# Optimization experiments

Hardware: AMD Instinct MI355X
Metric: run time of the kernel (lower is better)

The kernel has to match this reference:

```python
import jax, jax.numpy as jnp
import numpy as np

B, S, D, H, C = 64, 512, 768, 768, 5


def setup_inputs() -> dict:
    key = jax.random.key(0)
    ks = jax.random.split(key, 7)
    return {
        "hidden_states": jax.random.normal(ks[0], (B, S, D), jnp.float32),
        "mask": jnp.ones((B, S), dtype=bool),
        # Dense(hidden_size, relu)
        "W1": jax.random.normal(ks[1], (D, H), jnp.float32) * 0.02,
        "b1": jnp.zeros((H,), jnp.float32),
        # CRF inner dense -> potentials over num_classes
        "W2": jax.random.normal(ks[2], (H, C), jnp.float32) * 0.02,
        "b2": jnp.zeros((C,), jnp.float32),
        # CRF transition matrix and boundary energies (tfa use_boundary=True)
        "chain_kernel": jax.random.normal(ks[3], (C, C), jnp.float32) * 0.1,
        "left_boundary": jax.random.normal(ks[4], (C,), jnp.float32) * 0.1,
        "right_boundary": jax.random.normal(ks[5], (C,), jnp.float32) * 0.1,
    }


def viterbi_decode(potentials, trans):
    """potentials: [B,S,C], trans: [C,C] -> decoded tags [B,S] int32."""
    pot_t = jnp.swapaxes(potentials, 0, 1)  # [S,B,C]

    def fwd_step(alpha, pot):
        scores = alpha[:, :, None] + trans[None]      # [B,C_prev,C_cur]
        bp = jnp.argmax(scores, axis=1)               # [B,C]
        alpha = jnp.max(scores, axis=1) + pot         # [B,C]
        return alpha, bp

    alpha, bps = jax.lax.scan(fwd_step, pot_t[0], pot_t[1:])  # bps: [S-1,B,C]
    last = jnp.argmax(alpha, axis=-1).astype(jnp.int32)       # [B]

    def back_step(tag, bp):
        prev = jnp.take_along_axis(bp, tag[:, None], axis=1)[:, 0].astype(jnp.int32)
        return prev, prev

    _, tags = jax.lax.scan(back_step, last, bps, reverse=True)  # [S-1,B]
    decoded = jnp.concatenate([jnp.swapaxes(tags, 0, 1), last[:, None]], axis=1)
    return decoded


def reference(hidden_states, mask, W1, b1, W2, b2, chain_kernel,
              left_boundary, right_boundary):
    # Dense + ReLU (dropout is identity at inference / training=False)
    h = jax.nn.relu(jnp.einsum('bsd,dh->bsh', hidden_states, W1) + b1)
    # CRF inner dense -> unary potentials
    pot = jnp.einsum('bsh,hc->bsc', h, W2) + b2
    # boundary energies at first / last timestep (mask is full-length here)
    pot = pot.at[:, 0].add(left_boundary).at[:, -1].add(right_boundary)
    seq_length = jnp.sum(mask.astype(jnp.int32), axis=1)
    decoded = viterbi_decode(pot, chain_kernel)
    return decoded, pot, seq_length, chain_kernel
```

## Files before the change

### kernel.cpp

```cpp
#include <hip/hip_runtime.h>

#define B_  64
#define S_  512
#define D_  768
#define H_  768
#define C_  5
#define M_  (B_ * S_)

typedef float f32x4 __attribute__((ext_vector_type(4)));
typedef short short8 __attribute__((ext_vector_type(8)));

#define W1T_ELEMS (D_ * H_)
#define XBF_ELEMS (M_ * D_)

#define PX_BLOCKS   (XBF_ELEMS / (256 * 8))
#define PW_BLOCKS   ((D_ / 32) * (H_ / 32))
#define PI_BLOCKS   ((M_ * C_ + 255) / 256)

__device__ __forceinline__ unsigned short f2bf(float f) {
    unsigned int u = __float_as_uint(f);
    u += 0x7FFFu + ((u >> 16) & 1u);
    return (unsigned short)(u >> 16);
}

__global__ __launch_bounds__(256) void prep_all_kernel(
    const float* __restrict__ X, const float* __restrict__ W1,
    const float* __restrict__ b2, const float* __restrict__ lb,
    const float* __restrict__ rb,
    unsigned short* __restrict__ xbf, unsigned short* __restrict__ w1t,
    float* __restrict__ pot)
{
    __shared__ float t[32][33];
    const int bid = blockIdx.x;
    const int tid = threadIdx.x;

    if (bid < PX_BLOCKS) {
        const size_t i0 = ((size_t)bid * 256 + tid) * 8;
        const float4 a = *(const float4*)(X + i0);
        const float4 b = *(const float4*)(X + i0 + 4);
        union { unsigned short u[8]; uint4 v; } o;
        o.u[0] = f2bf(a.x); o.u[1] = f2bf(a.y); o.u[2] = f2bf(a.z); o.u[3] = f2bf(a.w);
        o.u[4] = f2bf(b.x); o.u[5] = f2bf(b.y); o.u[6] = f2bf(b.z); o.u[7] = f2bf(b.w);
        *(uint4*)(xbf + i0) = o.v;
    } else if (bid < PX_BLOCKS + PW_BLOCKS) {
        const int b2i = bid - PX_BLOCKS;
        const int bx = b2i % (H_ / 32);
        const int by = b2i / (H_ / 32);
        const int lx = tid & 31, ly = tid >> 5;
        #pragma unroll
        for (int j = 0; j < 4; ++j)
            t[ly + 8 * j][lx] = W1[(by * 32 + ly + 8 * j) * H_ + bx * 32 + lx];
        __syncthreads();
        #pragma unroll
        for (int j = 0; j < 4; ++j)
            w1t[(size_t)(bx * 32 + ly + 8 * j) * D_ + by * 32 + lx] = f2bf(t[lx][ly + 8 * j]);
    } else {
        const int idx = (bid - PX_BLOCKS - PW_BLOCKS) * 256 + tid;
        if (idx < M_ * C_) {
            const int c = idx % C_;
            const int tt = (idx / C_) & (S_ - 1);
            float v = b2[c];
            if (tt == 0)      v += lb[c];
            if (tt == S_ - 1) v += rb[c];
            pot[idx] = v;
        }
    }
}

__global__ __launch_bounds__(256) void prep_w1_kernel(
    const float* __restrict__ W1, unsigned short* __restrict__ w1t)
{
    __shared__ float t[32][33];
    const int bx = blockIdx.x, by = blockIdx.y;
    const int lx = threadIdx.x & 31, ly = threadIdx.x >> 5;
    #pragma unroll
    for (int j = 0; j < 4; ++j)
        t[ly + 8 * j][lx] = W1[(by * 32 + ly + 8 * j) * H_ + bx * 32 + lx];
    __syncthreads();
    #pragma unroll
    for (int j = 0; j < 4; ++j)
        w1t[(size_t)(bx * 32 + ly + 8 * j) * D_ + by * 32 + lx] = f2bf(t[lx][ly + 8 * j]);
}

__global__ __launch_bounds__(256) void init_pot_kernel(
    const float* __restrict__ b2, const float* __restrict__ lb,
    const float* __restrict__ rb, float* __restrict__ pot)
{
    const int idx = blockIdx.x * 256 + threadIdx.x;
    if (idx < M_ * C_) {
        const int c = idx % C_;
        const int t = (idx / C_) & (S_ - 1);
        float v = b2[c];
        if (t == 0)      v += lb[c];
        if (t == S_ - 1) v += rb[c];
        pot[idx] = v;
    }
}

__device__ __forceinline__ void gload16(const void* g, void* l) {
    __builtin_amdgcn_global_load_lds(
        (const __attribute__((address_space(1))) unsigned int*)g,
        (__attribute__((address_space(3))) unsigned int*)l, 16, 0, 0);
}

__global__ __launch_bounds__(256) void gemm_bk64_kernel(
    const unsigned short* __restrict__ xbf,
    const unsigned short* __restrict__ w1t,
    const float* __restrict__ b1,
    const float* __restrict__ W2,
    float* __restrict__ pot)
{
    __shared__ __align__(16) unsigned short Asm[2][8192];
    __shared__ __align__(16) unsigned short Bsm[2][8192];

    const int tid  = threadIdx.x;
    const int lane = tid & 63, w = tid >> 6;
    const int wm   = w >> 1, wn = w & 1;
    const int i15  = lane & 15, quad = lane >> 4;

    const int bid = blockIdx.x;
    const int r8 = bid & 7, q8 = bid >> 3;
    const int nb = q8 % 6, mhi = q8 / 6;
    const int m0 = (mhi * 8 + r8) * 128;
    const int n0 = nb * 128;

    const unsigned short* gA[2];
    const unsigned short* gB[2];
    int lofs[2];
    #pragma unroll
    for (int i = 0; i < 2; ++i) {
        const int g = 2 * w + i;
        gA[i] = xbf + (size_t)(m0 + g * 16 + i15) * D_ + quad * 8;
        gB[i] = w1t + (size_t)(n0 + g * 16 + i15) * D_ + quad * 8;
        lofs[i] = g * 512;
    }

    f32x4 acc[4][4];
    #pragma unroll
    for (int mi = 0; mi < 4; ++mi)
        #pragma unroll
        for (int ni = 0; ni < 4; ++ni)
            acc[mi][ni] = (f32x4){0.f, 0.f, 0.f, 0.f};

    #pragma unroll
    for (int i = 0; i < 2; ++i) {
        gload16(gA[i],      &Asm[0][lofs[i]]);
        gload16(gA[i] + 32, &Asm[0][4096 + lofs[i]]);
        gload16(gB[i],      &Bsm[0][lofs[i]]);
        gload16(gB[i] + 32, &Bsm[0][4096 + lofs[i]]);
        gA[i] += 64; gB[i] += 64;
    }
    __syncthreads();

    #define KITERS (D_ / 64)
    for (int kt = 0; kt < KITERS; ++kt) {
        const int cur = kt & 1, nxt = cur ^ 1;

        if (kt + 1 < KITERS) {
            #pragma unroll
            for (int i = 0; i < 2; ++i) {
                gload16(gA[i],      &Asm[nxt][lofs[i]]);
                gload16(gA[i] + 32, &Asm[nxt][4096 + lofs[i]]);
                gload16(gB[i],      &Bsm[nxt][lofs[i]]);
                gload16(gB[i] + 32, &Bsm[nxt][4096 + lofs[i]]);
                gA[i] += 64; gB[i] += 64;
            }
        }

        #pragma unroll
        for (int c = 0; c < 2; ++c) {
            const int cb = c * 4096;
            short8 af[4], bfr[4];
            #pragma unroll
            for (int mi = 0; mi < 4; ++mi)
                af[mi] = *(const short8*)&Asm[cur][cb + (wm * 4 + mi) * 512 + quad * 128 + i15 * 8];
            #pragma unroll
            for (int ni = 0; ni < 4; ++ni)
                bfr[ni] = *(const short8*)&Bsm[cur][cb + (wn * 4 + ni) * 512 + quad * 128 + i15 * 8];
            #pragma unroll
            for (int ni = 0; ni < 4; ++ni)
                #pragma unroll
                for (int mi = 0; mi < 4; ++mi)
                    acc[mi][ni] = __builtin_amdgcn_mfma_f32_16x16x32_bf16(
                        af[mi], bfr[ni], acc[mi][ni], 0, 0, 0);
        }

        __syncthreads();
    }

    float* pp = (float*)&Asm[0][0];

    float b1v[4], w2v[4][C_];
    #pragma unroll
    for (int ni = 0; ni < 4; ++ni) {
        const int col = n0 + wn * 64 + ni * 16 + i15;
        b1v[ni] = b1[col];
        #pragma unroll
        for (int cc = 0; cc < C_; ++cc) w2v[ni][cc] = W2[col * C_ + cc];
    }

    #pragma unroll
    for (int mi = 0; mi < 4; ++mi) {
        float ps[4][C_];
        #pragma unroll
        for (int r = 0; r < 4; ++r)
            #pragma unroll
            for (int cc = 0; cc < C_; ++cc) ps[r][cc] = 0.f;

        #pragma unroll
        for (int ni = 0; ni < 4; ++ni)
            #pragma unroll
            for (int r = 0; r < 4; ++r) {
                float h = acc[mi][ni][r] + b1v[ni];
                h = h > 0.f ? h : 0.f;
                #pragma unroll
                for (int cc = 0; cc < C_; ++cc)
                    ps[r][cc] = fmaf(h, w2v[ni][cc], ps[r][cc]);
            }

        #pragma unroll
        for (int off = 1; off < 16; off <<= 1)
            #pragma unroll
            for (int r = 0; r < 4; ++r)
                #pragma unroll
                for (int cc = 0; cc < C_; ++cc)
                    ps[r][cc] += __shfl_xor(ps[r][cc], off, 64);

        if (i15 == 0) {
            #pragma unroll
            for (int r = 0; r < 4; ++r) {
                const int row = wm * 64 + mi * 16 + quad * 4 + r;
                #pragma unroll
                for (int cc = 0; cc < C_; ++cc)
                    pp[(wn * 128 + row) * C_ + cc] = ps[r][cc];
            }
        }
    }
    __syncthreads();

    for (int idx = tid; idx < 128 * C_; idx += 256) {
        const int row = idx / C_, cc = idx % C_;
        atomicAdd(&pot[(size_t)(m0 + row) * C_ + cc],
                  pp[row * C_ + cc] + pp[(128 + row) * C_ + cc]);
    }
}

__global__ __launch_bounds__(256) void gemm_bf16_kernel(
    const float* __restrict__ X,
    const unsigned short* __restrict__ w1t,
    const float* __restrict__ b1,
    const float* __restrict__ W2,
    float* __restrict__ pot)
{
    __shared__ __align__(16) float          Asm[128 * 32];
    __shared__ __align__(16) unsigned short Bsm[128 * 32];
    __shared__ float pp[2][128][C_];

    const int tid  = threadIdx.x;
    const int lane = tid & 63, w = tid >> 6;
    const int wm   = w >> 1, wn = w & 1;
    const int i15  = lane & 15, quad = lane >> 4;

    const int bid = blockIdx.x;
    const int r8 = bid & 7, q8 = bid >> 3;
    const int nb = q8 % 6, mhi = q8 / 6;
    const int m0 = (mhi * 8 + r8) * 128;
    const int n0 = nb * 128;

    const float* gA[4];
    float* lA[4];
    const unsigned short* gB[2];
    unsigned short* lB[2];
    #pragma unroll
    for (int i = 0; i < 4; ++i) {
        const int a = 4 * w + i, g = a >> 1, h = a & 1;
        gA[i] = X + (size_t)(m0 + g * 16 + i15) * D_ + (4 * h + quad) * 4;
        lA[i] = &Asm[g * 512 + h * 256];
    }
    #pragma unroll
    for (int i = 0; i < 2; ++i) {
        const int b = 2 * w + i;
        gB[i] = w1t + (size_t)(n0 + b * 16 + i15) * D_ + quad * 8;
        lB[i] = &Bsm[b * 512];
    }

    f32x4 acc[4][4];
    #pragma unroll
    for (int mi = 0; mi < 4; ++mi)
        #pragma unroll
        for (int ni = 0; ni < 4; ++ni)
            acc[mi][ni] = (f32x4){0.f, 0.f, 0.f, 0.f};

    for (int kt = 0; kt < D_ / 32; ++kt) {
        __syncthreads();
        #pragma unroll
        for (int i = 0; i < 4; ++i) { gload16(gA[i], lA[i]); gA[i] += 32; }
        #pragma unroll
        for (int i = 0; i < 2; ++i) { gload16(gB[i], lB[i]); gB[i] += 32; }
        __syncthreads();

        short8 af[4];
        #pragma unroll
        for (int mi = 0; mi < 4; ++mi) {
            const int row = wm * 64 + mi * 16 + i15;
            const int base = (row >> 4) * 512 + (row & 15) * 4 + quad * 128;
            const f32x4 lo = *(const f32x4*)&Asm[base];
            const f32x4 hi = *(const f32x4*)&Asm[base + 64];
            float f[8];
            *(f32x4*)&f[0] = lo; *(f32x4*)&f[4] = hi;
            union { short8 s; unsigned short u[8]; } cv;
            #pragma unroll
            for (int j = 0; j < 8; ++j) cv.u[j] = f2bf(f[j]);
            af[mi] = cv.s;
        }
        short8 bfr[4];
        #pragma unroll
        for (int ni = 0; ni < 4; ++ni) {
            const int row = wn * 64 + ni * 16 + i15;
            bfr[ni] = *(const short8*)&Bsm[(row >> 4) * 512 + quad * 128 + (row & 15) * 8];
        }
        #pragma unroll
        for (int ni = 0; ni < 4; ++ni)
            #pragma unroll
            for (int mi = 0; mi < 4; ++mi)
                acc[mi][ni] = __builtin_amdgcn_mfma_f32_16x16x32_bf16(
                    af[mi], bfr[ni], acc[mi][ni], 0, 0, 0);
    }

    float b1v[4], w2v[4][C_];
    #pragma unroll
    for (int ni = 0; ni < 4; ++ni) {
        const int col = n0 + wn * 64 + ni * 16 + i15;
        b1v[ni] = b1[col];
        #pragma unroll
        for (int cc = 0; cc < C_; ++cc) w2v[ni][cc] = W2[col * C_ + cc];
    }

    #pragma unroll
    for (int mi = 0; mi < 4; ++mi) {
        float ps[4][C_];
        #pragma unroll
        for (int r = 0; r < 4; ++r)
            #pragma unroll
            for (int cc = 0; cc < C_; ++cc) ps[r][cc] = 0.f;

        #pragma unroll
        for (int ni = 0; ni < 4; ++ni)
            #pragma unroll
            for (int r = 0; r < 4; ++r) {
                float h = acc[mi][ni][r] + b1v[ni];
                h = h > 0.f ? h : 0.f;
                #pragma unroll
                for (int cc = 0; cc < C_; ++cc)
                    ps[r][cc] = fmaf(h, w2v[ni][cc], ps[r][cc]);
            }

        #pragma unroll
        for (int off = 1; off < 16; off <<= 1)
            #pragma unroll
            for (int r = 0; r < 4; ++r)
                #pragma unroll
                for (int cc = 0; cc < C_; ++cc)
                    ps[r][cc] += __shfl_xor(ps[r][cc], off, 64);

        if (i15 == 0) {
            #pragma unroll
            for (int r = 0; r < 4; ++r) {
                const int row = wm * 64 + mi * 16 + quad * 4 + r;
                #pragma unroll
                for (int cc = 0; cc < C_; ++cc)
                    pp[wn][row][cc] = ps[r][cc];
            }
        }
    }
    __syncthreads();

    for (int idx = tid; idx < 128 * C_; idx += 256) {
        const int row = idx / C_, cc = idx % C_;
        atomicAdd(&pot[(size_t)(m0 + row) * C_ + cc],
                  pp[0][row][cc] + pp[1][row][cc]);
    }
}

#define FBK 8
#define FLDS 132
__global__ __launch_bounds__(256) void gemm_relu_pot_kernel(
    const float* __restrict__ X, const float* __restrict__ W1,
    const float* __restrict__ b1, const float* __restrict__ W2,
    float* __restrict__ pot)
{
    __shared__ float As[FBK * FLDS];
    __shared__ float Bs[FBK * FLDS];
    __shared__ float w2s[128][C_];

    const int tid = threadIdx.x;
    const int tx = tid & 15, ty = tid >> 4;
    const int m0 = blockIdx.y * 128, n0 = blockIdx.x * 128;

    for (int idx = tid; idx < 128 * C_; idx += 256)
        w2s[idx / C_][idx % C_] = W2[(n0 + idx / C_) * C_ + idx % C_];

    float acc[2][2][4][4];
    #pragma unroll
    for (int a = 0; a < 2; ++a)
        #pragma unroll
        for (int b = 0; b < 2; ++b)
            #pragma unroll
            for (int i = 0; i < 4; ++i)
                #pragma unroll
                for (int j = 0; j < 4; ++j) acc[a][b][i][j] = 0.f;

    const int arow = tid >> 1, aq = tid & 1;
    const int brow = tid >> 5, bq = tid & 31;
    const float* Aptr = X + (m0 + arow) * D_ + aq * 4;
    const float* Bptr = W1 + brow * H_ + n0 + bq * 4;

    for (int kt = 0; kt < D_; kt += FBK) {
        const float4 avv = *(const float4*)Aptr;
        const float4 bvv = *(const float4*)Bptr;
        __syncthreads();
        As[(aq * 4 + 0) * FLDS + arow] = avv.x;
        As[(aq * 4 + 1) * FLDS + arow] = avv.y;
        As[(aq * 4 + 2) * FLDS + arow] = avv.z;
        As[(aq * 4 + 3) * FLDS + arow] = avv.w;
        *(float4*)&Bs[brow * FLDS + bq * 4] = bvv;
        __syncthreads();
        #pragma unroll
        for (int k = 0; k < FBK; ++k) {
            const float4 a0 = *(const float4*)&As[k * FLDS + (ty << 2)];
            const float4 a1 = *(const float4*)&As[k * FLDS + 64 + (ty << 2)];
            const float4 b0 = *(const float4*)&Bs[k * FLDS + (tx << 2)];
            const float4 b1r = *(const float4*)&Bs[k * FLDS + 64 + (tx << 2)];
            const float ar[2][4] = {{a0.x,a0.y,a0.z,a0.w},{a1.x,a1.y,a1.z,a1.w}};
            const float br[2][4] = {{b0.x,b0.y,b0.z,b0.w},{b1r.x,b1r.y,b1r.z,b1r.w}};
            #pragma unroll
            for (int ri = 0; ri < 2; ++ri)
                #pragma unroll
                for (int i = 0; i < 4; ++i)
                    #pragma unroll
                    for (int rj = 0; rj < 2; ++rj)
                        #pragma unroll
                        for (int j = 0; j < 4; ++j)
                            acc[ri][rj][i][j] = fmaf(ar[ri][i], br[rj][j], acc[ri][rj][i][j]);
        }
        Aptr += FBK;
        Bptr += FBK * H_;
    }

    float ps[2][4][C_];
    #pragma unroll
    for (int ri = 0; ri < 2; ++ri)
        #pragma unroll
        for (int i = 0; i < 4; ++i)
            #pragma unroll
            for (int cc = 0; cc < C_; ++cc) ps[ri][i][cc] = 0.f;

    #pragma unroll
    for (int rj = 0; rj < 2; ++rj)
        #pragma unroll
        for (int j = 0; j < 4; ++j) {
            const int nl = rj * 64 + (tx << 2) + j;
            const float bj = b1[n0 + nl];
            float w2c[C_];
            #pragma unroll
            for (int cc = 0; cc < C_; ++cc) w2c[cc] = w2s[nl][cc];
            #pragma unroll
            for (int ri = 0; ri < 2; ++ri)
                #pragma unroll
                for (int i = 0; i < 4; ++i) {
                    float h = acc[ri][rj][i][j] + bj;
                    h = h > 0.f ? h : 0.f;
                    #pragma unroll
                    for (int cc = 0; cc < C_; ++cc)
                        ps[ri][i][cc] = fmaf(h, w2c[cc], ps[ri][i][cc]);
                }
        }

    #pragma unroll
    for (int off = 1; off < 16; off <<= 1)
        #pragma unroll
        for (int ri = 0; ri < 2; ++ri)
            #pragma unroll
            for (int i = 0; i < 4; ++i)
                #pragma unroll
                for (int cc = 0; cc < C_; ++cc)
                    ps[ri][i][cc] += __shfl_xor(ps[ri][i][cc], off, 64);

    if (tx == 0)
        #pragma unroll
        for (int ri = 0; ri < 2; ++ri)
            #pragma unroll
            for (int i = 0; i < 4; ++i) {
                const int m = m0 + ri * 64 + (ty << 2) + i;
                #pragma unroll
                for (int cc = 0; cc < C_; ++cc)
                    atomicAdd(&pot[m * C_ + cc], ps[ri][i][cc]);
            }
}

__global__ __launch_bounds__(64) void viterbi_kernel(
    const float* __restrict__ pot, const float* __restrict__ trans,
    const int* __restrict__ mask, float* __restrict__ decoded,
    float* __restrict__ seqlen, float* __restrict__ chain_out)
{
    const int b = blockIdx.x;
    const int lane = threadIdx.x;

    __shared__ float pl[S_ * C_];
    __shared__ unsigned int bpk[S_];
    __shared__ unsigned int gseg[64];
    __shared__ int bt[64];
    __shared__ int dec_s[S_];
    __shared__ int s_last;

    const float* pb = pot + b * (S_ * C_);
    for (int i = lane; i < S_ * C_; i += 64) pl[i] = pb[i];

    int mcnt = 0;
    const int* mb = mask + b * S_;
    for (int i = lane; i < S_; i += 64) mcnt += (mb[i] != 0) ? 1 : 0;
    #pragma unroll
    for (int off = 32; off >= 1; off >>= 1) mcnt += __shfl_xor(mcnt, off, 64);

    if (b == 0 && lane < C_ * C_) chain_out[lane] = trans[lane];

    float tr[C_][C_];
    #pragma unroll
    for (int p = 0; p < C_; ++p)
        #pragma unroll
        for (int c = 0; c < C_; ++c) tr[p][c] = trans[p * C_ + c];

    __syncthreads();

    const float NEG = -1.0e30f;

    float G[C_][C_];
    #pragma unroll
    for (int c = 0; c < C_; ++c)
        #pragma unroll
        for (int p = 0; p < C_; ++p) G[c][p] = (c == p) ? 0.f : NEG;

    for (int j = 1; j <= 8; ++j) {
        const int t = 8 * lane + j;
        if (t < S_) {
            float ng[C_][C_];
            #pragma unroll
            for (int c = 0; c < C_; ++c) {
                const float pc = pl[t * C_ + c];
                #pragma unroll
                for (int p = 0; p < C_; ++p) {
                    float m = tr[0][c] + G[0][p];
                    #pragma unroll
                    for (int q = 1; q < C_; ++q)
                        m = fmaxf(m, tr[q][c] + G[q][p]);
                    ng[c][p] = m + pc;
                }
            }
            #pragma unroll
            for (int c = 0; c < C_; ++c)
                #pragma unroll
                for (int p = 0; p < C_; ++p) G[c][p] = ng[c][p];
        }
    }

    #pragma unroll
    for (int d = 1; d < 64; d <<= 1) {
        float Q[C_][C_];
        #pragma unroll
        for (int q = 0; q < C_; ++q)
            #pragma unroll
            for (int p = 0; p < C_; ++p) Q[q][p] = __shfl_up(G[q][p], d, 64);
        if (lane >= d) {
            float ng[C_][C_];
            #pragma unroll
            for (int c = 0; c < C_; ++c)
                #pragma unroll
                for (int p = 0; p < C_; ++p) {
                    float m = G[c][0] + Q[0][p];
                    #pragma unroll
                    for (int q = 1; q < C_; ++q)
                        m = fmaxf(m, G[c][q] + Q[q][p]);
                    ng[c][p] = m;
                }
            #pragma unroll
            for (int c = 0; c < C_; ++c)
                #pragma unroll
                for (int p = 0; p < C_; ++p) G[c][p] = ng[c][p];
        }
    }

    float a[C_];
    {
        float E[C_][C_];
        #pragma unroll
        for (int c = 0; c < C_; ++c)
            #pragma unroll
            for (int p = 0; p < C_; ++p) E[c][p] = __shfl_up(G[c][p], 1, 64);
        float a0[C_];
        #pragma unroll
        for (int c = 0; c < C_; ++c) a0[c] = pl[c];
        if (lane == 0) {
            #pragma unroll
            for (int c = 0; c < C_; ++c) a[c] = a0[c];
        } else {
            #pragma unroll
            for (int c = 0; c < C_; ++c) {
                float m = E[c][0] + a0[0];
                #pragma unroll
                for (int q = 1; q < C_; ++q) m = fmaxf(m, E[c][q] + a0[q]);
                a[c] = m;
            }
        }
    }

    for (int j = 1; j <= 8; ++j) {
        const int t = 8 * lane + j;
        if (t < S_) {
            unsigned int mpack = 0;
            float na[C_];
            #pragma unroll
            for (int c = 0; c < C_; ++c) {
                float best = a[0] + tr[0][c];
                int arg = 0;
                #pragma unroll
                for (int p = 1; p < C_; ++p) {
                    const float s = a[p] + tr[p][c];
                    if (s > best) { best = s; arg = p; }
                }
                mpack |= (unsigned int)arg << (3 * c);
                na[c] = best + pl[t * C_ + c];
            }
            bpk[t] = mpack;
            #pragma unroll
            for (int c = 0; c < C_; ++c) a[c] = na[c];
        }
    }

    if (lane == 63) {
        float best = a[0];
        int arg = 0;
        #pragma unroll
        for (int p = 1; p < C_; ++p)
            if (a[p] > best) { best = a[p]; arg = p; }
        s_last = arg;
    }
    if (lane == 0) bpk[0] = 0;
    __syncthreads();

    const int last = s_last;

    unsigned int g = 0u | (1u << 3) | (2u << 6) | (3u << 9) | (4u << 12);
    #pragma unroll
    for (int j = 7; j >= 0; --j) {
        const int t = 8 * lane + j;
        if (t >= 1) {
            const unsigned int m = bpk[t];
            unsigned int ng = 0;
            #pragma unroll
            for (int x = 0; x < C_; ++x) {
                const unsigned int gx = (g >> (3 * x)) & 7u;
                ng |= ((m >> (3 * gx)) & 7u) << (3 * x);
            }
            g = ng;
        }
    }
    gseg[lane] = g;
    __syncthreads();

    if (lane == 0) {
        int cur = last;
        for (int l = 63; l >= 0; --l) {
            bt[l] = cur;
            cur = (int)((gseg[l] >> (3 * cur)) & 7u);
        }
        seqlen[b] = (float)mcnt;
    }
    __syncthreads();

    {
        int tag = bt[lane];
        const int t0 = 8 * lane;
        dec_s[t0 + 7] = tag;
        #pragma unroll
        for (int t = t0 + 7; t >= t0 + 1; --t) {
            tag = (int)((bpk[t] >> (3 * tag)) & 7u);
            dec_s[t - 1] = tag;
        }
    }
    __syncthreads();

    float* db = decoded + b * S_;
    for (int i = lane; i < S_; i += 64) db[i] = (float)dec_s[i];
}

extern "C" void kernel_launch(void* const* d_in, const int* in_sizes, int n_in,
                              void* d_out, int out_size, void* d_ws, size_t ws_size,
                              hipStream_t stream) {
    const float* hs    = (const float*)d_in[0];
    const int*   mask  = (const int*)  d_in[1];
    const float* W1    = (const float*)d_in[2];
    const float* b1    = (const float*)d_in[3];
    const float* W2    = (const float*)d_in[4];
    const float* b2    = (const float*)d_in[5];
    const float* chain = (const float*)d_in[6];
    const float* lb    = (const float*)d_in[7];
    const float* rb    = (const float*)d_in[8];

    float* out      = (float*)d_out;
    float* decoded  = out;
    float* pot      = out + M_;
    float* seq      = out + M_ + M_ * C_;
    float* chainout = seq + B_;

    const size_t need_w1 = (size_t)W1T_ELEMS * sizeof(unsigned short);
    const size_t need_all = need_w1 + (size_t)XBF_ELEMS * sizeof(unsigned short);

    if (ws_size >= need_all) {
        unsigned short* w1t = (unsigned short*)d_ws;
        unsigned short* xbf = w1t + W1T_ELEMS;
        prep_all_kernel<<<PX_BLOCKS + PW_BLOCKS + PI_BLOCKS, 256, 0, stream>>>(
            hs, W1, b2, lb, rb, xbf, w1t, pot);
        gemm_bk64_kernel<<<1536, 256, 0, stream>>>(xbf, w1t, b1, W2, pot);
    } else if (ws_size >= need_w1) {
        unsigned short* w1t = (unsigned short*)d_ws;
        init_pot_kernel<<<PI_BLOCKS, 256, 0, stream>>>(b2, lb, rb, pot);
        dim3 pgrid(H_ / 32, D_ / 32);
        prep_w1_kernel<<<pgrid, 256, 0, stream>>>(W1, w1t);
        gemm_bf16_kernel<<<1536, 256, 0, stream>>>(hs, w1t, b1, W2, pot);
    } else {
        init_pot_kernel<<<PI_BLOCKS, 256, 0, stream>>>(b2, lb, rb, pot);
        dim3 grid(H_ / 128, M_ / 128);
        gemm_relu_pot_kernel<<<grid, 256, 0, stream>>>(hs, W1, b1, W2, pot);
    }

    viterbi_kernel<<<B_, 64, 0, stream>>>(pot, chain, mask, decoded, seq, chainout);
}
```

Before: 271.4 us.

## Replace 128x128 GEMM with 256x256 8-wave tile and phased prefetch schedule

```diff
diff --git a/kernel.cpp b/kernel.cpp
--- a/kernel.cpp
+++ b/kernel.cpp
@@ -103,92 +103,136 @@
         (__attribute__((address_space(3))) unsigned int*)l, 16, 0, 0);
 }
 
-__global__ __launch_bounds__(256) void gemm_bk64_kernel(
+#define KT_ (D_ / 64)
+
+#define PH_BAR() do { \
+    __builtin_amdgcn_sched_barrier(0); \
+    __builtin_amdgcn_s_barrier(); \
+    __builtin_amdgcn_sched_barrier(0); \
+} while (0)
+
+#define STG_A(BUF, KI, HH) do { \
+    gload16(aSrc + (size_t)(HH) * 128 * D_ + (KI) * 64,      &Alds[BUF][(((HH) * 8 + w) * 2 + 0) * 512]); \
+    gload16(aSrc + (size_t)(HH) * 128 * D_ + (KI) * 64 + 32, &Alds[BUF][(((HH) * 8 + w) * 2 + 1) * 512]); \
+} while (0)
+#define STG_B(BUF, KI, HH) do { \
+    gload16(bSrc + (size_t)(HH) * 128 * D_ + (KI) * 64,      &Blds[BUF][(((HH) * 8 + w) * 2 + 0) * 512]); \
+    gload16(bSrc + (size_t)(HH) * 128 * D_ + (KI) * 64 + 32, &Blds[BUF][(((HH) * 8 + w) * 2 + 1) * 512]); \
+} while (0)
+
+#define LDA(CUR, G16, KK) (*(const short8*)&Alds[CUR][((G16) * 2 + (KK)) * 512 + lane * 8])
+#define LDB(CUR, G16, KK) (*(const short8*)&Blds[CUR][((G16) * 2 + (KK)) * 512 + lane * 8])
+
+#define MFMA_Q(MH, NH, BR) do { \
+    __builtin_amdgcn_s_setprio(1); \
+    _Pragma("unroll") \
+    for (int kk = 0; kk < 2; ++kk) \
+        _Pragma("unroll") \
+        for (int n2 = 0; n2 < 2; ++n2) \
+            _Pragma("unroll") \
+            for (int m2 = 0; m2 < 4; ++m2) \
+                acc[(MH) * 4 + m2][(NH) * 2 + n2] = __builtin_amdgcn_mfma_f32_16x16x32_bf16( \
+                    af[m2][kk], BR[n2][kk], acc[(MH) * 4 + m2][(NH) * 2 + n2], 0, 0, 0); \
+    __builtin_amdgcn_s_setprio(0); \
+} while (0)
+
+#define TILE_BODY(KI, CUR, NXT, DO_S1, DO_S2, VMODE) do { \
+     \
+    _Pragma("unroll") \
+    for (int m2 = 0; m2 < 4; ++m2) { \
+        af[m2][0] = LDA(CUR, wm * 8 + m2, 0); \
+        af[m2][1] = LDA(CUR, wm * 8 + m2, 1); \
+    } \
+    _Pragma("unroll") \
+    for (int n2 = 0; n2 < 2; ++n2) { \
+        blo[n2][0] = LDB(CUR, wn * 4 + n2, 0); \
+        blo[n2][1] = LDB(CUR, wn * 4 + n2, 1); \
+    } \
+    if (DO_S1) { STG_B(NXT, (KI) + 1, 0); } \
+    PH_BAR(); \
+    MFMA_Q(0, 0, blo); \
+    PH_BAR(); \
+     \
+    _Pragma("unroll") \
+    for (int n2 = 0; n2 < 2; ++n2) { \
+        bhi[n2][0] = LDB(CUR, wn * 4 + 2 + n2, 0); \
+        bhi[n2][1] = LDB(CUR, wn * 4 + 2 + n2, 1); \
+    } \
+    if (DO_S2) { STG_A(CUR, (KI) + 2, 0); } \
+    PH_BAR(); \
+    MFMA_Q(0, 1, bhi); \
+    PH_BAR(); \
+     \
+    _Pragma("unroll") \
+    for (int m2 = 0; m2 < 4; ++m2) { \
+        af[m2][0] = LDA(CUR, wm * 8 + 4 + m2, 0); \
+        af[m2][1] = LDA(CUR, wm * 8 + 4 + m2, 1); \
+    } \
+    if (DO_S2) { STG_B(CUR, (KI) + 2, 1); } \
+    PH_BAR(); \
+    MFMA_Q(1, 1, bhi); \
+    PH_BAR(); \
+     \
+    if (DO_S2) { STG_A(CUR, (KI) + 2, 1); } \
+    PH_BAR(); \
+    MFMA_Q(1, 0, blo); \
+    if ((VMODE) == 6) { asm volatile("s_waitcnt vmcnt(6)" ::: "memory"); } \
+    else if ((VMODE) == 0) { asm volatile("s_waitcnt vmcnt(0)" ::: "memory"); } \
+    PH_BAR(); \
+} while (0)
+
+__global__ __launch_bounds__(512) void gemm_256_kernel(
     const unsigned short* __restrict__ xbf,
     const unsigned short* __restrict__ w1t,
     const float* __restrict__ b1,
     const float* __restrict__ W2,
     float* __restrict__ pot)
 {
-    __shared__ __align__(16) unsigned short Asm[2][8192];
-    __shared__ __align__(16) unsigned short Bsm[2][8192];
+    __shared__ __align__(16) unsigned short Alds[2][16384];
+    __shared__ __align__(16) unsigned short Blds[2][16384];
 
     const int tid  = threadIdx.x;
-    const int lane = tid & 63, w = tid >> 6;
-    const int wm   = w >> 1, wn = w & 1;
+    const int lane = tid & 63;
+    const int w    = tid >> 6;
+    const int wm   = w >> 2;
+    const int wn   = w & 3;
     const int i15  = lane & 15, quad = lane >> 4;
 
-    const int bid = blockIdx.x;
-    const int r8 = bid & 7, q8 = bid >> 3;
-    const int nb = q8 % 6, mhi = q8 / 6;
-    const int m0 = (mhi * 8 + r8) * 128;
-    const int n0 = nb * 128;
-
-    const unsigned short* gA[2];
-    const unsigned short* gB[2];
-    int lofs[2];
-    #pragma unroll
-    for (int i = 0; i < 2; ++i) {
-        const int g = 2 * w + i;
-        gA[i] = xbf + (size_t)(m0 + g * 16 + i15) * D_ + quad * 8;
-        gB[i] = w1t + (size_t)(n0 + g * 16 + i15) * D_ + quad * 8;
-        lofs[i] = g * 512;
-    }
-
-    f32x4 acc[4][4];
-    #pragma unroll
-    for (int mi = 0; mi < 4; ++mi)
+    const int bid  = blockIdx.x;
+    const int wgid = (bid & 7) * 48 + (bid >> 3);
+    const int nb   = wgid % 3, mb = wgid / 3;
+    const int m0   = mb * 256, n0 = nb * 256;
+
+    const unsigned short* aSrc = xbf + (size_t)(m0 + w * 16 + i15) * D_ + quad * 8;
+    const unsigned short* bSrc = w1t + (size_t)(n0 + w * 16 + i15) * D_ + quad * 8;
+
+    f32x4 acc[8][4];
+    #pragma unroll
+    for (int mi = 0; mi < 8; ++mi)
         #pragma unroll
         for (int ni = 0; ni < 4; ++ni)
             acc[mi][ni] = (f32x4){0.f, 0.f, 0.f, 0.f};
 
-    #pragma unroll
-    for (int i = 0; i < 2; ++i) {
-        gload16(gA[i],      &Asm[0][lofs[i]]);
-        gload16(gA[i] + 32, &Asm[0][4096 + lofs[i]]);
-        gload16(gB[i],      &Bsm[0][lofs[i]]);
-        gload16(gB[i] + 32, &Bsm[0][4096 + lofs[i]]);
-        gA[i] += 64; gB[i] += 64;
-    }
-    __syncthreads();
-
-    #define KITERS (D_ / 64)
-    for (int kt = 0; kt < KITERS; ++kt) {
-        const int cur = kt & 1, nxt = cur ^ 1;
-
-        if (kt + 1 < KITERS) {
-            #pragma unroll
-            for (int i = 0; i < 2; ++i) {
-                gload16(gA[i],      &Asm[nxt][lofs[i]]);
-                gload16(gA[i] + 32, &Asm[nxt][4096 + lofs[i]]);
-                gload16(gB[i],      &Bsm[nxt][lofs[i]]);
-                gload16(gB[i] + 32, &Bsm[nxt][4096 + lofs[i]]);
-                gA[i] += 64; gB[i] += 64;
-            }
-        }
-
-        #pragma unroll
-        for (int c = 0; c < 2; ++c) {
-            const int cb = c * 4096;
-            short8 af[4], bfr[4];
-            #pragma unroll
-            for (int mi = 0; mi < 4; ++mi)
-                af[mi] = *(const short8*)&Asm[cur][cb + (wm * 4 + mi) * 512 + quad * 128 + i15 * 8];
-            #pragma unroll
-            for (int ni = 0; ni < 4; ++ni)
-                bfr[ni] = *(const short8*)&Bsm[cur][cb + (wn * 4 + ni) * 512 + quad * 128 + i15 * 8];
-            #pragma unroll
-            for (int ni = 0; ni < 4; ++ni)
-                #pragma unroll
-                for (int mi = 0; mi < 4; ++mi)
-                    acc[mi][ni] = __builtin_amdgcn_mfma_f32_16x16x32_bf16(
-                        af[mi], bfr[ni], acc[mi][ni], 0, 0, 0);
-        }
-
-        __syncthreads();
-    }
-
-    float* pp = (float*)&Asm[0][0];
+    short8 af[4][2], blo[2][2], bhi[2][2];
+
+    STG_B(0, 0, 0);
+    STG_A(0, 0, 0);
+    STG_B(0, 0, 1);
+    STG_A(0, 0, 1);
+    STG_A(1, 1, 0);
+    STG_B(1, 1, 1);
+    STG_A(1, 1, 1);
+    asm volatile("s_waitcnt vmcnt(6)" ::: "memory");
+    PH_BAR();
+
+    for (int k = 0; k < 10; k += 2) {
+        TILE_BODY(k,     0, 1, 1, 1, 6);
+        TILE_BODY(k + 1, 1, 0, 1, 1, 6);
+    }
+    TILE_BODY(10, 0, 1, 1, 0, 0);
+    TILE_BODY(11, 1, 0, 0, 0, 2);
+
+    float* pp = (float*)&Alds[0][0];
 
     float b1v[4], w2v[4][C_];
     #pragma unroll
@@ -200,7 +244,7 @@
     }
 
     #pragma unroll
-    for (int mi = 0; mi < 4; ++mi) {
+    for (int mi = 0; mi < 8; ++mi) {
         float ps[4][C_];
         #pragma unroll
         for (int r = 0; r < 4; ++r)
@@ -229,19 +273,18 @@
         if (i15 == 0) {
             #pragma unroll
             for (int r = 0; r < 4; ++r) {
-                const int row = wm * 64 + mi * 16 + quad * 4 + r;
+                const int row = wm * 128 + mi * 16 + quad * 4 + r;
                 #pragma unroll
                 for (int cc = 0; cc < C_; ++cc)
-                    pp[(wn * 128 + row) * C_ + cc] = ps[r][cc];
+                    pp[(wn * 256 + row) * C_ + cc] = ps[r][cc];
             }
         }
     }
     __syncthreads();
 
-    for (int idx = tid; idx < 128 * C_; idx += 256) {
-        const int row = idx / C_, cc = idx % C_;
-        atomicAdd(&pot[(size_t)(m0 + row) * C_ + cc],
-                  pp[row * C_ + cc] + pp[(128 + row) * C_ + cc]);
+    for (int idx = tid; idx < 256 * C_; idx += 512) {
+        atomicAdd(&pot[(size_t)m0 * C_ + idx],
+                  pp[idx] + pp[256 * C_ + idx] + pp[2 * 256 * C_ + idx] + pp[3 * 256 * C_ + idx]);
     }
 }
 
@@ -720,7 +763,7 @@
         unsigned short* xbf = w1t + W1T_ELEMS;
         prep_all_kernel<<<PX_BLOCKS + PW_BLOCKS + PI_BLOCKS, 256, 0, stream>>>(
             hs, W1, b2, lb, rb, xbf, w1t, pot);
-        gemm_bk64_kernel<<<1536, 256, 0, stream>>>(xbf, w1t, b1, W2, pot);
+        gemm_256_kernel<<<384, 512, 0, stream>>>(xbf, w1t, b1, W2, pot);
     } else if (ws_size >= need_w1) {
         unsigned short* w1t = (unsigned short*)d_ws;
         init_pot_kernel<<<PI_BLOCKS, 256, 0, stream>>>(b2, lb, rb, pot);
```

After: 277.4 us. 2.2% more time.
